# Optimization experiments

Hardware: AMD Instinct MI355X
Metric: run time of the kernel (lower is better)

Reference implementation:

```python
import jax, jax.numpy as jnp
import numpy as np

L, B, D = 2048, 8, 768
EPS_BN = 1e-5
EPS_LN = 1e-5
SCALE = 1.0 / float(np.sqrt(D))


def setup_inputs() -> dict:
    key = jax.random.key(0)
    ks = jax.random.split(key, 8)
    f32 = jnp.float32
    return {
        "x_a": jax.random.normal(ks[0], (L, B, D), dtype=f32),
        "x_v": jax.random.normal(ks[1], (L, B, D), dtype=f32),
        "x": jax.random.normal(ks[2], (L, B, D), dtype=f32),
        # conv1x1 (audio branch): weight [out_ch, in_ch], bias [out_ch]
        "W_a": jax.random.normal(ks[3], (D, D), dtype=f32) * 0.02,
        "b_a": jnp.zeros((D,), f32),
        "bn_a_g": jnp.ones((D,), f32),
        "bn_a_b": jnp.zeros((D,), f32),
        "prelu_a": jnp.full((1,), 0.25, f32),
        # conv1x1 (video branch)
        "W_v": jax.random.normal(ks[4], (D, D), dtype=f32) * 0.02,
        "b_v": jnp.zeros((D,), f32),
        "bn_v_g": jnp.ones((D,), f32),
        "bn_v_b": jnp.zeros((D,), f32),
        "prelu_v": jnp.full((1,), 0.25, f32),
        # final LayerNorm affine
        "ln_g": jnp.ones((D,), f32),
        "ln_b": jnp.zeros((D,), f32),
    }


def _branch(q, kv, W, b, bn_g, bn_b, alpha):
    # q: [B, L, D] queries; kv: [B, Lm, D] keys == values (cross-modal)
    attn = jax.nn.softmax(jnp.einsum('bld,bmd->blm', q, kv) * SCALE, axis=-1)
    ctx = jnp.einsum('blm,bmd->bld', attn, kv)            # [B, L, D]
    # Conv1d(kernel=1) over channel dim D == per-position linear
    y = jnp.einsum('bld,ed->ble', ctx, W) + b             # [B, L, D]
    # BatchNorm1d in training mode: batch stats over (B, L) per channel, biased var
    mean = jnp.mean(y, axis=(0, 1))
    var = jnp.var(y, axis=(0, 1))
    y = (y - mean) * jax.lax.rsqrt(var + EPS_BN) * bn_g + bn_b
    # PReLU (single shared alpha)
    return jnp.where(y > 0, y, alpha * y)


def reference(x_a, x_v, x, W_a, b_a, bn_a_g, bn_a_b, prelu_a,
              W_v, b_v, bn_v_g, bn_v_b, prelu_v, ln_g, ln_b):
    xa = jnp.swapaxes(x_a, 0, 1)   # [B, La, D]
    xv = jnp.swapaxes(x_v, 0, 1)   # [B, Lv, D]
    xq = jnp.swapaxes(x, 0, 1)     # [B, L, D]

    res_a = _branch(xq, xa, W_a, b_a, bn_a_g, bn_a_b, prelu_a)
    res_v = _branch(xq, xv, W_v, b_v, bn_v_g, bn_v_b, prelu_v)

    out = xq + res_a + res_v
    out = jnp.swapaxes(out, 0, 1)  # back to [L, B, D]

    mu = jnp.mean(out, axis=-1, keepdims=True)
    var = jnp.var(out, axis=-1, keepdims=True)
    return (out - mu) * jax.lax.rsqrt(var + EPS_LN) * ln_g + ln_b
```

## Files before the change

kernel.cpp:

```cpp
#include <hip/hip_runtime.h>
#include <stdint.h>

#define LL 2048
#define BB 8
#define DD 768
#define NROWS (LL*BB)
#define QKSCALE 0.03608439182435161f
#define EP 72

typedef __attribute__((ext_vector_type(8))) short short8;
typedef __attribute__((ext_vector_type(4))) float f32x4;
typedef unsigned short u16;
typedef unsigned int u32;

__device__ __forceinline__ float bf2f(u16 u) {
    union { u32 u; float f; } c; c.u = ((u32)u) << 16; return c.f;
}
__device__ __forceinline__ u16 f2bf(float f) {
    union { float f; u32 u; } c; c.f = f;
    return (u16)((c.u + 0x8000u) >> 16);
}

__global__ __launch_bounds__(256)
void cvt_kernel(const float* __restrict__ s0, u16* __restrict__ d0,
                const float* __restrict__ s1, u16* __restrict__ d1,
                const float* __restrict__ s2, u16* __restrict__ d2,
                const float* __restrict__ s3, u16* __restrict__ d3,
                const float* __restrict__ s4, u16* __restrict__ d4,
                int nbig4, int nsmall4)
{
    const float* src; u16* dst; int n4;
    switch (blockIdx.y) {
        case 0: src = s0; dst = d0; n4 = nbig4; break;
        case 1: src = s1; dst = d1; n4 = nbig4; break;
        case 2: src = s2; dst = d2; n4 = nbig4; break;
        case 3: src = s3; dst = d3; n4 = nsmall4; break;
        default: src = s4; dst = d4; n4 = nsmall4; break;
    }
    for (int i = blockIdx.x * 256 + threadIdx.x; i < n4; i += gridDim.x * 256) {
        float4 v = *(const float4*)&src[i * 4];
        ushort4 o;
        o.x = f2bf(v.x); o.y = f2bf(v.y); o.z = f2bf(v.z); o.w = f2bf(v.w);
        *(ushort4*)&dst[i * 4] = o;
    }
}

template<int EPI>
__global__ __launch_bounds__(256)
void gemm_bt(const u16* __restrict__ A, int lda, long astr,
             const u16* __restrict__ B, int ldb, long bstr,
             u16* __restrict__ C, long cstr, int ldc,
             int K, int sw,
             float* __restrict__ lsum,
             const float* __restrict__ bias,
             float* __restrict__ stats)
{
    __shared__ u16 lds[18432];
    u16* As = lds;
    u16* Bs = lds + 8192;

    const int tid = threadIdx.x;
    const int z = blockIdx.z;
    const int flat = blockIdx.y * gridDim.x + blockIdx.x;
    const int per = sw * gridDim.x;
    const int bm = (flat / per) * sw + (flat % sw);
    const int bn = (flat % per) / sw;
    const int m0 = bm * 128, n0 = bn * 128;

    const u16* Ab = A + (size_t)z * astr + (size_t)m0 * lda;
    const u16* Bb = B + (size_t)z * bstr + (size_t)n0 * ldb;
    u16* Cb = C + (size_t)z * cstr;

    const int lane = tid & 63, w = tid >> 6;
    const int wm = w >> 1, wn = w & 1;
    const int lr = lane & 15, lg = lane >> 4;
    const int srow = lane >> 3;
    const int coff = ((lane & 7) ^ srow) * 8;

    f32x4 acc[4][4];
    const f32x4 zz = {0.f, 0.f, 0.f, 0.f};
    #pragma unroll
    for (int i = 0; i < 4; ++i)
        #pragma unroll
        for (int j = 0; j < 4; ++j) acc[i][j] = zz;

    for (int kt = 0; kt < K; kt += 64) {
        __syncthreads();
        #pragma unroll
        for (int p = 0; p < 4; ++p) {
            const int rb = w * 4 + p;
            const u16* ga = Ab + (size_t)(rb * 8 + srow) * lda + kt + coff;
            const u16* gb = Bb + (size_t)(rb * 8 + srow) * ldb + kt + coff;
            u16* la = As + rb * 512 + lane * 8;
            u16* lb = Bs + rb * 512 + lane * 8;
            __builtin_amdgcn_global_load_lds((const __attribute__((address_space(1))) u32*)ga,
                                             (__attribute__((address_space(3))) u32*)la,
                                             16, 0, 0);
            __builtin_amdgcn_global_load_lds((const __attribute__((address_space(1))) u32*)gb,
                                             (__attribute__((address_space(3))) u32*)lb,
                                             16, 0, 0);
        }
        __syncthreads();
        #pragma unroll
        for (int ks = 0; ks < 2; ++ks) {
            short8 af[4], bf[4];
            #pragma unroll
            for (int mi = 0; mi < 4; ++mi)
                af[mi] = *(const short8*)&As[(wm * 64 + mi * 16 + lr) * 64 + (((ks * 4 + lg) ^ (lr & 7)) * 8)];
            #pragma unroll
            for (int ni = 0; ni < 4; ++ni)
                bf[ni] = *(const short8*)&Bs[(wn * 64 + ni * 16 + lr) * 64 + (((ks * 4 + lg) ^ (lr & 7)) * 8)];
            #pragma unroll
            for (int mi = 0; mi < 4; ++mi)
                #pragma unroll
                for (int ni = 0; ni < 4; ++ni)
                    acc[mi][ni] = __builtin_amdgcn_mfma_f32_16x16x32_bf16(af[mi], bf[ni], acc[mi][ni], 0, 0, 0);
        }
    }

    __syncthreads();
    u16* eb = lds + w * (64 * EP);

    float invl[4][4]; float bcol[4];
    if constexpr (EPI == 2) {
        #pragma unroll
        for (int mi = 0; mi < 4; ++mi)
            #pragma unroll
            for (int r = 0; r < 4; ++r)
                invl[mi][r] = 1.0f / lsum[z * 2048 + m0 + wm * 64 + mi * 16 + lg * 4 + r];
        #pragma unroll
        for (int ni = 0; ni < 4; ++ni)
            bcol[ni] = bias[n0 + wn * 64 + ni * 16 + lr];
    }
    float csum[4] = {0, 0, 0, 0}, csq[4] = {0, 0, 0, 0};

    #pragma unroll
    for (int mi = 0; mi < 4; ++mi) {
        float rsum[4] = {0, 0, 0, 0};
        #pragma unroll
        for (int ni = 0; ni < 4; ++ni) {
            #pragma unroll
            for (int r = 0; r < 4; ++r) {
                float v = acc[mi][ni][r];
                if constexpr (EPI == 1) { v = __expf(v * QKSCALE); rsum[r] += v; }
                if constexpr (EPI == 2) { v = v * invl[mi][r] + bcol[ni]; csum[ni] += v; csq[ni] += v * v; }
                eb[(mi * 16 + lg * 4 + r) * EP + ni * 16 + lr] = f2bf(v);
            }
        }
        if constexpr (EPI == 1) {
            #pragma unroll
            for (int r = 0; r < 4; ++r) {
                float s = rsum[r];
                s += __shfl_xor(s, 1); s += __shfl_xor(s, 2);
                s += __shfl_xor(s, 4); s += __shfl_xor(s, 8);
                if (lr == 0)
                    atomicAdd(&lsum[z * 2048 + m0 + wm * 64 + mi * 16 + lg * 4 + r], s);
            }
        }
    }
    if constexpr (EPI == 2) {
        #pragma unroll
        for (int ni = 0; ni < 4; ++ni) {
            float s = csum[ni], q = csq[ni];
            s += __shfl_xor(s, 16); s += __shfl_xor(s, 32);
            q += __shfl_xor(q, 16); q += __shfl_xor(q, 32);
            if (lg == 0) {
                atomicAdd(&stats[n0 + wn * 64 + ni * 16 + lr], s);
                atomicAdd(&stats[DD + n0 + wn * 64 + ni * 16 + lr], q);
            }
        }
    }
    __syncthreads();
    #pragma unroll
    for (int c = 0; c < 8; ++c) {
        int row = c * 8 + (lane >> 3);
        short8 v = *(const short8*)&eb[row * EP + (lane & 7) * 8];
        *(short8*)&Cb[(size_t)(m0 + wm * 64 + row) * ldc + n0 + wn * 64 + (lane & 7) * 8] = v;
    }
}

__global__ void bn_params(const float* __restrict__ stats_a, const float* __restrict__ stats_v,
                          const float* __restrict__ g_a, const float* __restrict__ be_a,
                          const float* __restrict__ g_v, const float* __restrict__ be_v,
                          float* __restrict__ bnp_a, float* __restrict__ bnp_v)
{
    const int e = threadIdx.x;
    const float* st = (blockIdx.x == 0) ? stats_a : stats_v;
    const float* g  = (blockIdx.x == 0) ? g_a  : g_v;
    const float* be = (blockIdx.x == 0) ? be_a : be_v;
    float* bnp = (blockIdx.x == 0) ? bnp_a : bnp_v;
    float mean = st[e] * (1.0f / NROWS);
    float var  = st[DD + e] * (1.0f / NROWS) - mean * mean;
    float scale = g[e] * rsqrtf(var + 1e-5f);
    bnp[e]      = scale;
    bnp[DD + e] = be[e] - mean * scale;
}

__global__ __launch_bounds__(256)
void final_kernel(const float* __restrict__ x,
                  const u16* __restrict__ y_a, const u16* __restrict__ y_v,
                  const float* __restrict__ bnp_a, const float* __restrict__ bnp_v,
                  const float* __restrict__ pra, const float* __restrict__ prv,
                  const float* __restrict__ lng, const float* __restrict__ lnb,
                  float* __restrict__ out)
{
    const int n = blockIdx.x;
    const int tid = threadIdx.x;
    __shared__ float vrow[DD];
    __shared__ float reds[4], reds2[4];
    const float aa = pra[0];
    const float av = prv[0];
    const size_t base = (size_t)n * DD;
    float s = 0.f, s2 = 0.f;
    for (int e = tid; e < DD; e += 256) {
        float ya = bf2f(y_a[base + e]) * bnp_a[e] + bnp_a[DD + e];
        ya = ya > 0.f ? ya : aa * ya;
        float yv = bf2f(y_v[base + e]) * bnp_v[e] + bnp_v[DD + e];
        yv = yv > 0.f ? yv : av * yv;
        float v = x[base + e] + ya + yv;
        vrow[e] = v;
        s += v; s2 += v * v;
    }
    for (int off = 32; off > 0; off >>= 1) { s += __shfl_xor(s, off); s2 += __shfl_xor(s2, off); }
    const int wv = tid >> 6;
    if ((tid & 63) == 0) { reds[wv] = s; reds2[wv] = s2; }
    __syncthreads();
    float ts  = reds[0] + reds[1] + reds[2] + reds[3];
    float ts2 = reds2[0] + reds2[1] + reds2[2] + reds2[3];
    float mean = ts * (1.0f / DD);
    float var  = ts2 * (1.0f / DD) - mean * mean;
    float rstd = rsqrtf(var + 1e-5f);
    for (int e = tid; e < DD; e += 256) {
        float o = (vrow[e] - mean) * rstd * lng[e] + lnb[e];
        out[base + e] = o;
    }
}

extern "C" void kernel_launch(void* const* d_in, const int* in_sizes, int n_in,
                              void* d_out, int out_size, void* d_ws, size_t ws_size,
                              hipStream_t stream)
{
    const float* x_a    = (const float*)d_in[0];
    const float* x_v    = (const float*)d_in[1];
    const float* x      = (const float*)d_in[2];
    const float* W_a    = (const float*)d_in[3];
    const float* b_a    = (const float*)d_in[4];
    const float* bn_a_g = (const float*)d_in[5];
    const float* bn_a_b = (const float*)d_in[6];
    const float* pr_a   = (const float*)d_in[7];
    const float* W_v    = (const float*)d_in[8];
    const float* b_v    = (const float*)d_in[9];
    const float* bn_v_g = (const float*)d_in[10];
    const float* bn_v_b = (const float*)d_in[11];
    const float* pr_v   = (const float*)d_in[12];
    const float* ln_g   = (const float*)d_in[13];
    const float* ln_b   = (const float*)d_in[14];

    float* stats_a = (float*)d_ws;
    float* stats_v = stats_a + 1536;
    float* bnp_a   = stats_v + 1536;
    float* bnp_v   = bnp_a + 1536;
    float* lsum    = bnp_v + 1536;
    u16* xq_bf = (u16*)(lsum + 16 * 2048);
    u16* xa_bf = xq_bf + (size_t)NROWS * DD;
    u16* xv_bf = xa_bf + (size_t)NROWS * DD;
    u16* Wa_bf = xv_bf + (size_t)NROWS * DD;
    u16* Wv_bf = Wa_bf + (size_t)DD * DD;
    u16* UT    = Wv_bf + (size_t)DD * DD;
    u16* y_a = xa_bf;
    u16* y_v = xv_bf;
    size_t fixed_bytes = (size_t)((char*)UT - (char*)d_ws);

    int nb = 1;
    for (int cand = 8; cand >= 1; cand >>= 1) {
        size_t need = fixed_bytes + (size_t)cand * (3145728ull + 8388608ull);
        if (need <= ws_size) { nb = cand; break; }
    }
    u16* P = UT + (size_t)nb * (768 * 2048);

    hipMemsetAsync(stats_a, 0, (3072 + 4 * 1536 - 3072 + 16 * 2048) * 0 + (3072 + 16 * 2048 + 3072) * sizeof(float), stream);

    cvt_kernel<<<dim3(3072, 5), 256, 0, stream>>>(
        x, xq_bf, x_a, xa_bf, x_v, xv_bf, W_a, Wa_bf, W_v, Wv_bf,
        NROWS * DD / 4, DD * DD / 4);

    const u16*   KVs[2]   = { xa_bf, xv_bf };
    const u16*   Ws[2]    = { Wa_bf, Wv_bf };
    const float* BIs[2]   = { b_a, b_v };
    u16*         Ys[2]    = { y_a, y_v };
    float*       STs[2]   = { stats_a, stats_v };

    for (int br = 0; br < 2; ++br) {
        const u16* kv = KVs[br];
        for (int c0 = 0; c0 < 8; c0 += nb) {
            float* lsum_bc = (nb == 8) ? (lsum + br * 8 * 2048) : lsum;
            if (nb != 8)
                hipMemsetAsync(lsum, 0, (size_t)nb * 2048 * sizeof(float), stream);
            gemm_bt<0><<<dim3(16, 6, nb), 256, 0, stream>>>(
                Ws[br], DD, 0, kv + c0 * DD, BB * DD, DD,
                UT, (long)768 * 2048, 2048, DD, 2, nullptr, nullptr, nullptr);
            gemm_bt<1><<<dim3(16, 16, nb), 256, 0, stream>>>(
                xq_bf + c0 * DD, BB * DD, DD, kv + c0 * DD, BB * DD, DD,
                P, (long)2048 * 2048, 2048, DD, 4, lsum_bc, nullptr, nullptr);
            gemm_bt<2><<<dim3(6, 16, nb), 256, 0, stream>>>(
                P, 2048, (long)2048 * 2048, UT, 2048, (long)768 * 2048,
                Ys[br] + (size_t)c0 * DD, DD, BB * DD, 2048, 4, lsum_bc, BIs[br], STs[br]);
        }
    }

    bn_params<<<2, 768, 0, stream>>>(stats_a, stats_v, bn_a_g, bn_a_b, bn_v_g, bn_v_b, bnp_a, bnp_v);
    final_kernel<<<NROWS, 256, 0, stream>>>(x, y_a, y_v, bnp_a, bnp_v, pr_a, pr_v, ln_g, ln_b,
                                            (float*)d_out);
}
```

Before: 590.8 us.

## Replace 128x128 GEMM with 256x256 tile, 4-stage LDS pipeline, 8 waves

Replaces the 128x128 single-buffered GEMM kernel with a 256x256-tile, 512-thread version. It uses a 4-slot LDS ring holding K=32 slices and prefetches two stages ahead with async global->LDS loads. Barriers are split around MFMA halves, with s_setprio raised during MFMA bursts, so loads overlap compute and global traffic per FLOP drops. The epilogue is written in two 64-row halves through a per-wave staging buffer. The risks are a larger register footprint, lower occupancy, and fewer blocks for the small UT GEMM (24 per batch), which may underfill the CUs.

Result: faster. 539.3 us (-8.7%).

```diff
diff --git a/kernel.cpp b/kernel.cpp
--- a/kernel.cpp
+++ b/kernel.cpp
@@ -45,19 +45,22 @@
     }
 }
 
+__device__ __forceinline__ void gll16(const u16* g, u16* l) {
+    __builtin_amdgcn_global_load_lds((const __attribute__((address_space(1))) u32*)g,
+                                     (__attribute__((address_space(3))) u32*)l, 16, 0, 0);
+}
+
 template<int EPI>
-__global__ __launch_bounds__(256)
-void gemm_bt(const u16* __restrict__ A, int lda, long astr,
-             const u16* __restrict__ B, int ldb, long bstr,
-             u16* __restrict__ C, long cstr, int ldc,
-             int K, int sw,
-             float* __restrict__ lsum,
-             const float* __restrict__ bias,
-             float* __restrict__ stats)
-{
-    __shared__ u16 lds[18432];
-    u16* As = lds;
-    u16* Bs = lds + 8192;
+__global__ __launch_bounds__(512, 2)
+void gemm_bt256(const u16* __restrict__ A, int lda, long astr,
+                const u16* __restrict__ B, int ldb, long bstr,
+                u16* __restrict__ C, long cstr, int ldc,
+                int K, int sw,
+                float* __restrict__ lsum,
+                const float* __restrict__ bias,
+                float* __restrict__ stats)
+{
+    __shared__ u16 lds[65536];
 
     const int tid = threadIdx.x;
     const int z = blockIdx.z;
@@ -65,69 +68,99 @@
     const int per = sw * gridDim.x;
     const int bm = (flat / per) * sw + (flat % sw);
     const int bn = (flat % per) / sw;
-    const int m0 = bm * 128, n0 = bn * 128;
+    const int m0 = bm * 256, n0 = bn * 256;
 
     const u16* Ab = A + (size_t)z * astr + (size_t)m0 * lda;
     const u16* Bb = B + (size_t)z * bstr + (size_t)n0 * ldb;
     u16* Cb = C + (size_t)z * cstr;
 
     const int lane = tid & 63, w = tid >> 6;
-    const int wm = w >> 1, wn = w & 1;
+    const int wm = w >> 2, wn = w & 3;
     const int lr = lane & 15, lg = lane >> 4;
-    const int srow = lane >> 3;
-    const int coff = ((lane & 7) ^ srow) * 8;
-
-    f32x4 acc[4][4];
+
+    const int ar0 = tid >> 2;
+    const int ar1 = ar0 + 128;
+    const int ag0 = (tid & 3) ^ ((ar0 >> 1) & 3);
+    const int ag1 = (tid & 3) ^ ((ar1 >> 1) & 3);
+    const u16* gA0 = Ab + (size_t)ar0 * lda + ag0 * 8;
+    const u16* gA1 = Ab + (size_t)ar1 * lda + ag1 * 8;
+    const u16* gB0 = Bb + (size_t)ar0 * ldb + ag0 * 8;
+    const u16* gB1 = Bb + (size_t)ar1 * ldb + ag1 * 8;
+    const int lA0 = tid * 8;
+    const int lA1 = tid * 8 + 4096;
+    const int lB0 = 8192 + tid * 8;
+    const int lB1 = 12288 + tid * 8;
+
+    const int swz = (lr >> 1) & 3;
+    const int aoff = (wm * 128 + lr) * 32 + ((lg ^ swz) * 8);
+    const int boff = 8192 + (wn * 64 + lr) * 32 + ((lg ^ swz) * 8);
+
+    f32x4 acc[8][4];
     const f32x4 zz = {0.f, 0.f, 0.f, 0.f};
     #pragma unroll
-    for (int i = 0; i < 4; ++i)
+    for (int i = 0; i < 8; ++i)
         #pragma unroll
         for (int j = 0; j < 4; ++j) acc[i][j] = zz;
 
-    for (int kt = 0; kt < K; kt += 64) {
-        __syncthreads();
-        #pragma unroll
-        for (int p = 0; p < 4; ++p) {
-            const int rb = w * 4 + p;
-            const u16* ga = Ab + (size_t)(rb * 8 + srow) * lda + kt + coff;
-            const u16* gb = Bb + (size_t)(rb * 8 + srow) * ldb + kt + coff;
-            u16* la = As + rb * 512 + lane * 8;
-            u16* lb = Bs + rb * 512 + lane * 8;
-            __builtin_amdgcn_global_load_lds((const __attribute__((address_space(1))) u32*)ga,
-                                             (__attribute__((address_space(3))) u32*)la,
-                                             16, 0, 0);
-            __builtin_amdgcn_global_load_lds((const __attribute__((address_space(1))) u32*)gb,
-                                             (__attribute__((address_space(3))) u32*)lb,
-                                             16, 0, 0);
-        }
-        __syncthreads();
-        #pragma unroll
-        for (int ks = 0; ks < 2; ++ks) {
-            short8 af[4], bf[4];
-            #pragma unroll
-            for (int mi = 0; mi < 4; ++mi)
-                af[mi] = *(const short8*)&As[(wm * 64 + mi * 16 + lr) * 64 + (((ks * 4 + lg) ^ (lr & 7)) * 8)];
+    const int nt = K >> 5;
+
+    {
+        u16* b0 = lds;
+        u16* b1 = lds + 16384;
+        gll16(gA0, b0 + lA0); gll16(gA1, b0 + lA1);
+        gll16(gB0, b0 + lB0); gll16(gB1, b0 + lB1);
+        gll16(gA0 + 32, b1 + lA0); gll16(gA1 + 32, b1 + lA1);
+        gll16(gB0 + 32, b1 + lB0); gll16(gB1 + 32, b1 + lB1);
+    }
+    asm volatile("s_waitcnt vmcnt(4)" ::: "memory");
+    asm volatile("s_barrier" ::: "memory");
+
+    for (int t = 0; t < nt; ++t) {
+        const int cb = (t & 3) * 16384;
+        const int sb = ((t + 2) & 3) * 16384;
+        const int kt2 = (t + 2) * 32;
+        const bool pre = (t + 2 < nt);
+        short8 af[4], bf[4];
+
+        #pragma unroll
+        for (int mi = 0; mi < 4; ++mi) af[mi] = *(const short8*)&lds[cb + aoff + mi * 512];
+        #pragma unroll
+        for (int ni = 0; ni < 4; ++ni) bf[ni] = *(const short8*)&lds[cb + boff + ni * 512];
+        if (pre) { gll16(gA0 + kt2, lds + sb + lA0); gll16(gA1 + kt2, lds + sb + lA1); }
+        asm volatile("s_barrier" ::: "memory");
+        __builtin_amdgcn_s_setprio(1);
+        #pragma unroll
+        for (int mi = 0; mi < 4; ++mi)
             #pragma unroll
             for (int ni = 0; ni < 4; ++ni)
-                bf[ni] = *(const short8*)&Bs[(wn * 64 + ni * 16 + lr) * 64 + (((ks * 4 + lg) ^ (lr & 7)) * 8)];
-            #pragma unroll
-            for (int mi = 0; mi < 4; ++mi)
-                #pragma unroll
-                for (int ni = 0; ni < 4; ++ni)
-                    acc[mi][ni] = __builtin_amdgcn_mfma_f32_16x16x32_bf16(af[mi], bf[ni], acc[mi][ni], 0, 0, 0);
-        }
-    }
-
-    __syncthreads();
-    u16* eb = lds + w * (64 * EP);
-
-    float invl[4][4]; float bcol[4];
-    if constexpr (EPI == 2) {
+                acc[mi][ni] = __builtin_amdgcn_mfma_f32_16x16x32_bf16(af[mi], bf[ni], acc[mi][ni], 0, 0, 0);
+        __builtin_amdgcn_s_setprio(0);
+
+        #pragma unroll
+        for (int mi = 0; mi < 4; ++mi) af[mi] = *(const short8*)&lds[cb + aoff + 2048 + mi * 512];
+        if (pre) { gll16(gB0 + kt2, lds + sb + lB0); gll16(gB1 + kt2, lds + sb + lB1); }
+        if (t < nt - 2) asm volatile("s_waitcnt vmcnt(4)" ::: "memory");
+        else            asm volatile("s_waitcnt vmcnt(0)" ::: "memory");
+        asm volatile("s_barrier" ::: "memory");
+        __builtin_amdgcn_s_setprio(1);
         #pragma unroll
         for (int mi = 0; mi < 4; ++mi)
             #pragma unroll
+            for (int ni = 0; ni < 4; ++ni)
+                acc[mi + 4][ni] = __builtin_amdgcn_mfma_f32_16x16x32_bf16(af[mi], bf[ni], acc[mi + 4][ni], 0, 0, 0);
+        __builtin_amdgcn_s_setprio(0);
+    }
+
+    asm volatile("s_barrier" ::: "memory");
+    u16* eb = lds + w * 4608;
+
+    float invl[8][4]; float bcol[4];
+    if constexpr (EPI == 2) {
+        #pragma unroll
+        for (int mi = 0; mi < 8; ++mi)
+            #pragma unroll
             for (int r = 0; r < 4; ++r)
-                invl[mi][r] = 1.0f / lsum[z * 2048 + m0 + wm * 64 + mi * 16 + lg * 4 + r];
+                invl[mi][r] = 1.0f / lsum[z * 2048 + m0 + wm * 128 + mi * 16 + lg * 4 + r];
         #pragma unroll
         for (int ni = 0; ni < 4; ++ni)
             bcol[ni] = bias[n0 + wn * 64 + ni * 16 + lr];
@@ -135,27 +168,37 @@
     float csum[4] = {0, 0, 0, 0}, csq[4] = {0, 0, 0, 0};
 
     #pragma unroll
-    for (int mi = 0; mi < 4; ++mi) {
-        float rsum[4] = {0, 0, 0, 0};
-        #pragma unroll
-        for (int ni = 0; ni < 4; ++ni) {
+    for (int half = 0; half < 2; ++half) {
+        #pragma unroll
+        for (int mi = 0; mi < 4; ++mi) {
+            const int MI = half * 4 + mi;
+            float rsum[4] = {0, 0, 0, 0};
             #pragma unroll
-            for (int r = 0; r < 4; ++r) {
-                float v = acc[mi][ni][r];
-                if constexpr (EPI == 1) { v = __expf(v * QKSCALE); rsum[r] += v; }
-                if constexpr (EPI == 2) { v = v * invl[mi][r] + bcol[ni]; csum[ni] += v; csq[ni] += v * v; }
-                eb[(mi * 16 + lg * 4 + r) * EP + ni * 16 + lr] = f2bf(v);
+            for (int ni = 0; ni < 4; ++ni) {
+                #pragma unroll
+                for (int r = 0; r < 4; ++r) {
+                    float v = acc[MI][ni][r];
+                    if constexpr (EPI == 1) { v = __expf(v * QKSCALE); rsum[r] += v; }
+                    if constexpr (EPI == 2) { v = v * invl[MI][r] + bcol[ni]; csum[ni] += v; csq[ni] += v * v; }
+                    eb[(mi * 16 + lg * 4 + r) * EP + ni * 16 + lr] = f2bf(v);
+                }
+            }
+            if constexpr (EPI == 1) {
+                #pragma unroll
+                for (int r = 0; r < 4; ++r) {
+                    float s = rsum[r];
+                    s += __shfl_xor(s, 1); s += __shfl_xor(s, 2);
+                    s += __shfl_xor(s, 4); s += __shfl_xor(s, 8);
+                    if (lr == 0)
+                        atomicAdd(&lsum[z * 2048 + m0 + wm * 128 + MI * 16 + lg * 4 + r], s);
+                }
             }
         }
-        if constexpr (EPI == 1) {
-            #pragma unroll
-            for (int r = 0; r < 4; ++r) {
-                float s = rsum[r];
-                s += __shfl_xor(s, 1); s += __shfl_xor(s, 2);
-                s += __shfl_xor(s, 4); s += __shfl_xor(s, 8);
-                if (lr == 0)
-                    atomicAdd(&lsum[z * 2048 + m0 + wm * 64 + mi * 16 + lg * 4 + r], s);
-            }
+        #pragma unroll
+        for (int c = 0; c < 8; ++c) {
+            int row = c * 8 + (lane >> 3);
+            short8 v = *(const short8*)&eb[row * EP + (lane & 7) * 8];
+            *(short8*)&Cb[(size_t)(m0 + wm * 128 + half * 64 + row) * ldc + n0 + wn * 64 + (lane & 7) * 8] = v;
         }
     }
     if constexpr (EPI == 2) {
@@ -169,13 +212,6 @@
                 atomicAdd(&stats[DD + n0 + wn * 64 + ni * 16 + lr], q);
             }
         }
-    }
-    __syncthreads();
-    #pragma unroll
-    for (int c = 0; c < 8; ++c) {
-        int row = c * 8 + (lane >> 3);
-        short8 v = *(const short8*)&eb[row * EP + (lane & 7) * 8];
-        *(short8*)&Cb[(size_t)(m0 + wm * 64 + row) * ldc + n0 + wn * 64 + (lane & 7) * 8] = v;
     }
 }
 
@@ -278,7 +314,7 @@
     }
     u16* P = UT + (size_t)nb * (768 * 2048);
 
-    hipMemsetAsync(stats_a, 0, (3072 + 4 * 1536 - 3072 + 16 * 2048) * 0 + (3072 + 16 * 2048 + 3072) * sizeof(float), stream);
+    hipMemsetAsync(stats_a, 0, (4 * 1536 + 16 * 2048) * sizeof(float), stream);
 
     cvt_kernel<<<dim3(3072, 5), 256, 0, stream>>>(
         x, xq_bf, x_a, xa_bf, x_v, xv_bf, W_a, Wa_bf, W_v, Wv_bf,
@@ -296,13 +332,13 @@
             float* lsum_bc = (nb == 8) ? (lsum + br * 8 * 2048) : lsum;
             if (nb != 8)
                 hipMemsetAsync(lsum, 0, (size_t)nb * 2048 * sizeof(float), stream);
-            gemm_bt<0><<<dim3(16, 6, nb), 256, 0, stream>>>(
+            gemm_bt256<0><<<dim3(8, 3, nb), 512, 0, stream>>>(
                 Ws[br], DD, 0, kv + c0 * DD, BB * DD, DD,
-                UT, (long)768 * 2048, 2048, DD, 2, nullptr, nullptr, nullptr);
-            gemm_bt<1><<<dim3(16, 16, nb), 256, 0, stream>>>(
+                UT, (long)768 * 2048, 2048, DD, 3, nullptr, nullptr, nullptr);
+            gemm_bt256<1><<<dim3(8, 8, nb), 512, 0, stream>>>(
                 xq_bf + c0 * DD, BB * DD, DD, kv + c0 * DD, BB * DD, DD,
                 P, (long)2048 * 2048, 2048, DD, 4, lsum_bc, nullptr, nullptr);
-            gemm_bt<2><<<dim3(6, 16, nb), 256, 0, stream>>>(
+            gemm_bt256<2><<<dim3(3, 8, nb), 512, 0, stream>>>(
                 P, 2048, (long)2048 * 2048, UT, 2048, (long)768 * 2048,
                 Ys[br] + (size_t)c0 * DD, DD, BB * DD, 2048, 4, lsum_bc, BIs[br], STs[br]);
         }
```
